# Performance work log

Hardware: AMD Instinct MI355X
Metric: run time of the kernel (lower is better)

The kernel has to match this reference:

```python
import jax, jax.numpy as jnp
import numpy as np

B, K, P, T = 4096, 128, 64, 4

def setup_inputs() -> dict:
    key = jax.random.key(0)
    ks = jax.random.split(key, 9)
    s = lambda k, shp: jax.random.normal(k, shp, dtype=jnp.float32) * 0.1
    return {
        "x": jax.random.normal(ks[0], (B, K, 1), dtype=jnp.float32),
        "w": jax.random.normal(ks[1], (B, K, 1), dtype=jnp.float32),
        "W1": s(ks[2], (P, 1)),   # theta_1: 1 -> p
        "W2": s(ks[3], (P, P)),   # theta_2: p -> p
        "W3": s(ks[4], (P, P)),   # theta_3: p -> p
        "W4": s(ks[5], (P, 1)),   # theta_4: 1 -> p
        "W5": s(ks[6], (1, 2 * P)),  # theta_5: 2p -> 1
        "W6": s(ks[7], (P, P)),   # theta_6: p -> p
        "W7": s(ks[8], (P, P)),   # theta_7: p -> p
    }


def reference(x, w, W1, W2, W3, W4, W5, W6, W7):
    # x, w: (B, K, 1). torch Linear(in,out,bias=False): y = v @ W.T, W: (out,in)
    b, k, _ = x.shape
    p = W1.shape[0]
    # per-node feature messages (invariant across T iterations in original code)
    tmsg = jax.nn.relu(jnp.einsum('bki,pi->bkp', w, W4))   # relu(theta_4(w_k)), (B,K,p)
    sum_t = tmsg.sum(axis=1, keepdims=True)                # (B,1,p)
    xmsg = jnp.einsum('bki,pi->bkp', x, W1)                # theta_1(x_k), (B,K,p)
    mu = jnp.zeros((b, k, p), dtype=x.dtype)
    for _ in range(T):
        sum_mu = mu.sum(axis=1, keepdims=True)             # (B,1,p)
        mu = jax.nn.relu(
            xmsg
            + jnp.einsum('bkp,qp->bkq', sum_mu - mu, W2)   # theta_2(sum_mu - mu_k)
            + jnp.einsum('bkp,qp->bkq', sum_t - tmsg, W3)  # theta_3(sum_t - t_k)
        )
    pooled = jax.nn.relu(jnp.einsum('bp,qp->bq', mu.sum(axis=1), W6))  # (B,p)
    local = jnp.einsum('bkp,qp->bkq', mu, W7)                           # (B,K,p)
    # theta_5(concat(relu(theta_6(pool)), theta_7(mu_k))); split W5 = [W5a | W5b]
    W5a, W5b = W5[:, :p], W5[:, p:]
    q = jnp.einsum('bp,op->bo', pooled, W5a)[:, None, :] + jnp.einsum('bkp,op->bko', local, W5b)
    return q  # (B, K, 1)
```

## Files before the change

### kernel.cpp

```cpp
#include <hip/hip_runtime.h>

typedef __bf16 bf16;
typedef __bf16 bf16x4 __attribute__((ext_vector_type(4)));
typedef __bf16 bf16x8 __attribute__((ext_vector_type(8)));
typedef float  f32x4  __attribute__((ext_vector_type(4)));

#define MFMA16(a, b, c) __builtin_amdgcn_mfma_f32_16x16x32_bf16((a), (b), (c), 0, 0, 0)

__global__ __launch_bounds__(64, 2)
void qnet_kernel(const float* __restrict__ Xg, const float* __restrict__ Wg,
                 const float* __restrict__ W1g, const float* __restrict__ W2g,
                 const float* __restrict__ W3g, const float* __restrict__ W4g,
                 const float* __restrict__ W5g, const float* __restrict__ W6g,
                 const float* __restrict__ W7g, float* __restrict__ Outg)
{
    __shared__ __align__(16) bf16 muS[128 * 64];
    __shared__ __align__(16) float uS[64];
    __shared__ __align__(16) float smS[64];

    const int lane = threadIdx.x;
    const int b    = blockIdx.x;
    const int l15  = lane & 15;
    const int quad = lane >> 4;
    const int sw   = l15 & 7;

    float xv0 = Xg[b * 128 + lane], xv1 = Xg[b * 128 + 64 + lane];
    float wv0 = Wg[b * 128 + lane], wv1 = Wg[b * 128 + 64 + lane];

    float Ap = fmaxf(wv0, 0.f) + fmaxf(wv1, 0.f);
    float Bn = fmaxf(-wv0, 0.f) + fmaxf(-wv1, 0.f);
#pragma unroll
    for (int m = 1; m < 64; m <<= 1) { Ap += __shfl_xor(Ap, m); Bn += __shfl_xor(Bn, m); }

    float xk[8], apk[8], bnk[8];
#pragma unroll
    for (int kt = 0; kt < 8; ++kt) {
        const int src = (kt & 3) * 16 + l15;
        float xs_ = (kt < 4) ? __shfl(xv0, src) : __shfl(xv1, src);
        float ws_ = (kt < 4) ? __shfl(wv0, src) : __shfl(wv1, src);
        xk[kt]  = xs_;
        apk[kt] = Ap - fmaxf(ws_, 0.f);
        bnk[kt] = Bn - fmaxf(-ws_, 0.f);
    }

    float sp = 0.f, sm = 0.f;
#pragma unroll
    for (int c = 0; c < 16; ++c) {
        f32x4 w4 = *(const f32x4*)&W4g[c * 4];
        f32x4 w3 = *(const f32x4*)&W3g[lane * 64 + c * 4];
#pragma unroll
        for (int e = 0; e < 4; ++e) {
            sp += fmaxf(w4[e], 0.f) * w3[e];
            sm += fmaxf(-w4[e], 0.f) * w3[e];
        }
    }
    float w1C[16], v3pC[16], v3mC[16];
#pragma unroll
    for (int qt = 0; qt < 4; ++qt) {
        f32x4 w1v = *(const f32x4*)&W1g[qt * 16 + quad * 4];
#pragma unroll
        for (int e = 0; e < 4; ++e) {
            const int q = qt * 16 + quad * 4 + e;
            v3pC[qt * 4 + e] = __shfl(sp, q);
            v3mC[qt * 4 + e] = __shfl(sm, q);
            w1C[qt * 4 + e]  = w1v[e];
        }
    }

    {
        float u = 0.f;
#pragma unroll
        for (int c = 0; c < 16; ++c) {
            f32x4 w5v = *(const f32x4*)&W5g[64 + c * 4];
#pragma unroll
            for (int e = 0; e < 4; ++e) u += w5v[e] * W7g[(c * 4 + e) * 64 + lane];
        }
        uS[lane] = u;
    }

    bf16x8 w2h[4][2], w2l[4][2];
#pragma unroll
    for (int qt = 0; qt < 4; ++qt)
#pragma unroll
        for (int s = 0; s < 2; ++s) {
            const float* src = &W2g[(qt * 16 + l15) * 64 + s * 32 + quad * 8];
            f32x4 f0 = *(const f32x4*)src;
            f32x4 f1 = *(const f32x4*)(src + 4);
            bf16x8 h, l;
#pragma unroll
            for (int e = 0; e < 4; ++e) {
                bf16 h0 = (bf16)f0[e], h1 = (bf16)f1[e];
                h[e] = h0; h[4 + e] = h1;
                l[e]     = (bf16)(f0[e] - (float)h0);
                l[4 + e] = (bf16)(f1[e] - (float)h1);
            }
            w2h[qt][s] = h; w2l[qt][s] = l;
        }

#pragma unroll
    for (int kt = 0; kt < 8; ++kt) {
        const int row = (kt * 16 + l15) * 64;
#pragma unroll
        for (int qt = 0; qt < 4; ++qt) {
            bf16x4 h;
#pragma unroll
            for (int e = 0; e < 4; ++e) {
                float t = fmaf(xk[kt], w1C[qt * 4 + e],
                          fmaf(apk[kt], v3pC[qt * 4 + e], bnk[kt] * v3mC[qt * 4 + e]));
                h[e] = (bf16)fmaxf(t, 0.f);
            }
            *(bf16x4*)&muS[row + ((2 * qt + (quad >> 1)) ^ sw) * 8 + 4 * (quad & 1)] = h;
        }
    }

    const f32x4 zero4 = {0.f, 0.f, 0.f, 0.f};
    float smv[16];
#pragma unroll
    for (int i = 0; i < 16; ++i) smv[i] = 0.f;

    for (int it = 0; it < 3; ++it) {
        f32x4 rs[4] = {zero4, zero4, zero4, zero4};
#pragma unroll
        for (int kt = 0; kt < 8; ++kt) {
            const int row = (kt * 16 + l15) * 64;
            bf16x8 m0 = *(const bf16x8*)&muS[row + ((quad) ^ sw) * 8];
            bf16x8 m1 = *(const bf16x8*)&muS[row + ((4 + quad) ^ sw) * 8];
#pragma unroll
            for (int qt = 0; qt < 4; ++qt) {
                f32x4 a = MFMA16(w2h[qt][0], m0, zero4);
                a = MFMA16(w2h[qt][1], m1, a);
                f32x4 c = MFMA16(w2l[qt][0], m0, zero4);
                c = MFMA16(w2l[qt][1], m1, c);
                rs[qt] += a + c;
            }
        }
#pragma unroll
        for (int m = 1; m <= 8; m <<= 1)
#pragma unroll
            for (int qt = 0; qt < 4; ++qt)
#pragma unroll
                for (int e = 0; e < 4; ++e)
                    rs[qt][e] += __shfl_xor(rs[qt][e], m);

#pragma unroll
        for (int kt = 0; kt < 8; ++kt) {
            const int row = (kt * 16 + l15) * 64;
            bf16x8 m0 = *(const bf16x8*)&muS[row + ((quad) ^ sw) * 8];
            bf16x8 m1 = *(const bf16x8*)&muS[row + ((4 + quad) ^ sw) * 8];
#pragma unroll
            for (int qt = 0; qt < 4; ++qt) {
                f32x4 a = MFMA16(w2h[qt][0], m0, zero4);
                a = MFMA16(w2h[qt][1], m1, a);
                bf16x4 h;
#pragma unroll
                for (int e = 0; e < 4; ++e) {
                    float t = fmaf(xk[kt], w1C[qt * 4 + e], rs[qt][e]);
                    t = fmaf(apk[kt], v3pC[qt * 4 + e], t);
                    t = fmaf(bnk[kt], v3mC[qt * 4 + e], t);
                    float v = fmaxf(t - a[e], 0.f);
                    h[e] = (bf16)v;
                    if (it == 2) smv[qt * 4 + e] += v;
                }
                *(bf16x4*)&muS[row + ((2 * qt + (quad >> 1)) ^ sw) * 8 + 4 * (quad & 1)] = h;
            }
        }
    }

#pragma unroll
    for (int m = 1; m <= 8; m <<= 1)
#pragma unroll
        for (int i = 0; i < 16; ++i) smv[i] += __shfl_xor(smv[i], m);
    if (l15 == 0) {
#pragma unroll
        for (int qt = 0; qt < 4; ++qt) {
            f32x4 v = {smv[qt * 4], smv[qt * 4 + 1], smv[qt * 4 + 2], smv[qt * 4 + 3]};
            *(f32x4*)&smS[qt * 16 + quad * 4] = v;
        }
    }

    float pl = 0.f;
#pragma unroll
    for (int c = 0; c < 16; ++c) {
        f32x4 sv = *(const f32x4*)&smS[c * 4];
        f32x4 w6 = *(const f32x4*)&W6g[lane * 64 + c * 4];
#pragma unroll
        for (int e = 0; e < 4; ++e) pl = fmaf(sv[e], w6[e], pl);
    }
    float qa = fmaxf(pl, 0.f) * W5g[lane];
#pragma unroll
    for (int m = 1; m < 64; m <<= 1) qa += __shfl_xor(qa, m);

    f32x4 uf[2][2];
#pragma unroll
    for (int s = 0; s < 2; ++s) {
        uf[s][0] = *(const f32x4*)&uS[s * 32 + quad * 8];
        uf[s][1] = *(const f32x4*)&uS[s * 32 + quad * 8 + 4];
    }

    float res[8];
#pragma unroll
    for (int kt = 0; kt < 8; ++kt) {
        const int row = (kt * 16 + l15) * 64;
        bf16x8 m0 = *(const bf16x8*)&muS[row + ((quad) ^ sw) * 8];
        bf16x8 m1 = *(const bf16x8*)&muS[row + ((4 + quad) ^ sw) * 8];
        float r = 0.f;
#pragma unroll
        for (int j = 0; j < 4; ++j) {
            r = fmaf((float)m0[j],     uf[0][0][j], r);
            r = fmaf((float)m0[4 + j], uf[0][1][j], r);
            r = fmaf((float)m1[j],     uf[1][0][j], r);
            r = fmaf((float)m1[4 + j], uf[1][1][j], r);
        }
        r += __shfl_xor(r, 16); r += __shfl_xor(r, 32);
        res[kt] = r;
    }
    float rA0 = (quad & 1) ? res[1] : res[0];
    float rA1 = (quad & 1) ? res[3] : res[2];
    float rA  = (quad & 2) ? rA1 : rA0;
    float rB0 = (quad & 1) ? res[5] : res[4];
    float rB1 = (quad & 1) ? res[7] : res[6];
    float rB  = (quad & 2) ? rB1 : rB0;
    Outg[b * 128 + lane]      = qa + rA;
    Outg[b * 128 + 64 + lane] = qa + rB;
}

extern "C" void kernel_launch(void* const* d_in, const int* in_sizes, int n_in,
                              void* d_out, int out_size, void* d_ws, size_t ws_size,
                              hipStream_t stream) {
    (void)n_in; (void)d_ws; (void)ws_size; (void)out_size;
    const int B = in_sizes[0] >> 7;
    qnet_kernel<<<B, 64, 0, stream>>>(
        (const float*)d_in[0], (const float*)d_in[1], (const float*)d_in[2],
        (const float*)d_in[3], (const float*)d_in[4], (const float*)d_in[5],
        (const float*)d_in[6], (const float*)d_in[7], (const float*)d_in[8],
        (float*)d_out);
}
```

Before: 136.3 us.

## Process two batch elements per wavefront to amortize weight setup and interleave MFMAs

Each single-wavefront block now handles two batch items. The per-block weight preprocessing (W2 hi/lo split into registers, W3/W4 folds, W7·W5b vector) is paid once per pair, and the MFMA chains for the two items are interleaved to expose more independent work. The cost is double the LDS use per block, more live registers, and half as many blocks, which reduces the wavefronts available to hide latency. Launch bounds are relaxed to allow the larger register footprint, and the launch assumes B is even.

```diff
diff --git a/kernel.cpp b/kernel.cpp
--- a/kernel.cpp
+++ b/kernel.cpp
@@ -7,40 +7,42 @@
 
 #define MFMA16(a, b, c) __builtin_amdgcn_mfma_f32_16x16x32_bf16((a), (b), (c), 0, 0, 0)
 
-__global__ __launch_bounds__(64, 2)
+__global__ __launch_bounds__(64, 1)
 void qnet_kernel(const float* __restrict__ Xg, const float* __restrict__ Wg,
                  const float* __restrict__ W1g, const float* __restrict__ W2g,
                  const float* __restrict__ W3g, const float* __restrict__ W4g,
                  const float* __restrict__ W5g, const float* __restrict__ W6g,
                  const float* __restrict__ W7g, float* __restrict__ Outg)
 {
-    __shared__ __align__(16) bf16 muS[128 * 64];
+    __shared__ __align__(16) bf16 muS[2][128 * 64];
     __shared__ __align__(16) float uS[64];
-    __shared__ __align__(16) float smS[64];
+    __shared__ __align__(16) float smS[2][64];
 
     const int lane = threadIdx.x;
-    const int b    = blockIdx.x;
+    const int b0   = blockIdx.x * 2;
     const int l15  = lane & 15;
     const int quad = lane >> 4;
     const int sw   = l15 & 7;
 
-    float xv0 = Xg[b * 128 + lane], xv1 = Xg[b * 128 + 64 + lane];
-    float wv0 = Wg[b * 128 + lane], wv1 = Wg[b * 128 + 64 + lane];
-
-    float Ap = fmaxf(wv0, 0.f) + fmaxf(wv1, 0.f);
-    float Bn = fmaxf(-wv0, 0.f) + fmaxf(-wv1, 0.f);
-#pragma unroll
-    for (int m = 1; m < 64; m <<= 1) { Ap += __shfl_xor(Ap, m); Bn += __shfl_xor(Bn, m); }
-
-    float xk[8], apk[8], bnk[8];
-#pragma unroll
-    for (int kt = 0; kt < 8; ++kt) {
-        const int src = (kt & 3) * 16 + l15;
-        float xs_ = (kt < 4) ? __shfl(xv0, src) : __shfl(xv1, src);
-        float ws_ = (kt < 4) ? __shfl(wv0, src) : __shfl(wv1, src);
-        xk[kt]  = xs_;
-        apk[kt] = Ap - fmaxf(ws_, 0.f);
-        bnk[kt] = Bn - fmaxf(-ws_, 0.f);
+    float xk[2][8], apk[2][8], bnk[2][8];
+#pragma unroll
+    for (int u = 0; u < 2; ++u) {
+        const int b = b0 + u;
+        float xv0 = Xg[b * 128 + lane], xv1 = Xg[b * 128 + 64 + lane];
+        float wv0 = Wg[b * 128 + lane], wv1 = Wg[b * 128 + 64 + lane];
+        float Ap = fmaxf(wv0, 0.f) + fmaxf(wv1, 0.f);
+        float Bn = fmaxf(-wv0, 0.f) + fmaxf(-wv1, 0.f);
+#pragma unroll
+        for (int m = 1; m < 64; m <<= 1) { Ap += __shfl_xor(Ap, m); Bn += __shfl_xor(Bn, m); }
+#pragma unroll
+        for (int kt = 0; kt < 8; ++kt) {
+            const int src = (kt & 3) * 16 + l15;
+            float xs_ = (kt < 4) ? __shfl(xv0, src) : __shfl(xv1, src);
+            float ws_ = (kt < 4) ? __shfl(wv0, src) : __shfl(wv1, src);
+            xk[u][kt]  = xs_;
+            apk[u][kt] = Ap - fmaxf(ws_, 0.f);
+            bnk[u][kt] = Bn - fmaxf(-ws_, 0.f);
+        }
     }
 
     float sp = 0.f, sm = 0.f;
@@ -101,37 +103,44 @@
     for (int kt = 0; kt < 8; ++kt) {
         const int row = (kt * 16 + l15) * 64;
 #pragma unroll
-        for (int qt = 0; qt < 4; ++qt) {
-            bf16x4 h;
-#pragma unroll
-            for (int e = 0; e < 4; ++e) {
-                float t = fmaf(xk[kt], w1C[qt * 4 + e],
-                          fmaf(apk[kt], v3pC[qt * 4 + e], bnk[kt] * v3mC[qt * 4 + e]));
-                h[e] = (bf16)fmaxf(t, 0.f);
-            }
-            *(bf16x4*)&muS[row + ((2 * qt + (quad >> 1)) ^ sw) * 8 + 4 * (quad & 1)] = h;
-        }
+        for (int u = 0; u < 2; ++u)
+#pragma unroll
+            for (int qt = 0; qt < 4; ++qt) {
+                bf16x4 h;
+#pragma unroll
+                for (int e = 0; e < 4; ++e) {
+                    float t = fmaf(xk[u][kt], w1C[qt * 4 + e],
+                              fmaf(apk[u][kt], v3pC[qt * 4 + e], bnk[u][kt] * v3mC[qt * 4 + e]));
+                    h[e] = (bf16)fmaxf(t, 0.f);
+                }
+                *(bf16x4*)&muS[u][row + ((2 * qt + (quad >> 1)) ^ sw) * 8 + 4 * (quad & 1)] = h;
+            }
     }
 
     const f32x4 zero4 = {0.f, 0.f, 0.f, 0.f};
-    float smv[16];
-#pragma unroll
-    for (int i = 0; i < 16; ++i) smv[i] = 0.f;
-
+    float smv[2][16];
     for (int it = 0; it < 3; ++it) {
-        f32x4 rs[4] = {zero4, zero4, zero4, zero4};
+        f32x4 rs0[4] = {zero4, zero4, zero4, zero4};
+        f32x4 rs1[4] = {zero4, zero4, zero4, zero4};
 #pragma unroll
         for (int kt = 0; kt < 8; ++kt) {
             const int row = (kt * 16 + l15) * 64;
-            bf16x8 m0 = *(const bf16x8*)&muS[row + ((quad) ^ sw) * 8];
-            bf16x8 m1 = *(const bf16x8*)&muS[row + ((4 + quad) ^ sw) * 8];
-#pragma unroll
-            for (int qt = 0; qt < 4; ++qt) {
-                f32x4 a = MFMA16(w2h[qt][0], m0, zero4);
-                a = MFMA16(w2h[qt][1], m1, a);
-                f32x4 c = MFMA16(w2l[qt][0], m0, zero4);
-                c = MFMA16(w2l[qt][1], m1, c);
-                rs[qt] += a + c;
+            bf16x8 a0 = *(const bf16x8*)&muS[0][row + ((quad) ^ sw) * 8];
+            bf16x8 a1 = *(const bf16x8*)&muS[0][row + ((4 + quad) ^ sw) * 8];
+            bf16x8 b0v = *(const bf16x8*)&muS[1][row + ((quad) ^ sw) * 8];
+            bf16x8 b1v = *(const bf16x8*)&muS[1][row + ((4 + quad) ^ sw) * 8];
+#pragma unroll
+            for (int qt = 0; qt < 4; ++qt) {
+                f32x4 pa = MFMA16(w2h[qt][0], a0, zero4);
+                pa = MFMA16(w2h[qt][1], a1, pa);
+                f32x4 qa_ = MFMA16(w2l[qt][0], a0, zero4);
+                qa_ = MFMA16(w2l[qt][1], a1, qa_);
+                rs0[qt] += pa + qa_;
+                f32x4 pb = MFMA16(w2h[qt][0], b0v, zero4);
+                pb = MFMA16(w2h[qt][1], b1v, pb);
+                f32x4 qb = MFMA16(w2l[qt][0], b0v, zero4);
+                qb = MFMA16(w2l[qt][1], b1v, qb);
+                rs1[qt] += pb + qb;
             }
         }
 #pragma unroll
@@ -139,29 +148,42 @@
 #pragma unroll
             for (int qt = 0; qt < 4; ++qt)
 #pragma unroll
-                for (int e = 0; e < 4; ++e)
-                    rs[qt][e] += __shfl_xor(rs[qt][e], m);
+                for (int e = 0; e < 4; ++e) {
+                    rs0[qt][e] += __shfl_xor(rs0[qt][e], m);
+                    rs1[qt][e] += __shfl_xor(rs1[qt][e], m);
+                }
 
 #pragma unroll
         for (int kt = 0; kt < 8; ++kt) {
             const int row = (kt * 16 + l15) * 64;
-            bf16x8 m0 = *(const bf16x8*)&muS[row + ((quad) ^ sw) * 8];
-            bf16x8 m1 = *(const bf16x8*)&muS[row + ((4 + quad) ^ sw) * 8];
-#pragma unroll
-            for (int qt = 0; qt < 4; ++qt) {
-                f32x4 a = MFMA16(w2h[qt][0], m0, zero4);
-                a = MFMA16(w2h[qt][1], m1, a);
-                bf16x4 h;
+            bf16x8 a0 = *(const bf16x8*)&muS[0][row + ((quad) ^ sw) * 8];
+            bf16x8 a1 = *(const bf16x8*)&muS[0][row + ((4 + quad) ^ sw) * 8];
+            bf16x8 b0v = *(const bf16x8*)&muS[1][row + ((quad) ^ sw) * 8];
+            bf16x8 b1v = *(const bf16x8*)&muS[1][row + ((4 + quad) ^ sw) * 8];
+#pragma unroll
+            for (int qt = 0; qt < 4; ++qt) {
+                f32x4 aa = MFMA16(w2h[qt][0], a0, zero4);
+                aa = MFMA16(w2h[qt][1], a1, aa);
+                f32x4 ab = MFMA16(w2h[qt][0], b0v, zero4);
+                ab = MFMA16(w2h[qt][1], b1v, ab);
+                bf16x4 ha, hb;
 #pragma unroll
                 for (int e = 0; e < 4; ++e) {
-                    float t = fmaf(xk[kt], w1C[qt * 4 + e], rs[qt][e]);
-                    t = fmaf(apk[kt], v3pC[qt * 4 + e], t);
-                    t = fmaf(bnk[kt], v3mC[qt * 4 + e], t);
-                    float v = fmaxf(t - a[e], 0.f);
-                    h[e] = (bf16)v;
-                    if (it == 2) smv[qt * 4 + e] += v;
+                    float t = fmaf(xk[0][kt], w1C[qt * 4 + e], rs0[qt][e]);
+                    t = fmaf(apk[0][kt], v3pC[qt * 4 + e], t);
+                    t = fmaf(bnk[0][kt], v3mC[qt * 4 + e], t);
+                    float v = fmaxf(t - aa[e], 0.f);
+                    ha[e] = (bf16)v;
+                    float t2 = fmaf(xk[1][kt], w1C[qt * 4 + e], rs1[qt][e]);
+                    t2 = fmaf(apk[1][kt], v3pC[qt * 4 + e], t2);
+                    t2 = fmaf(bnk[1][kt], v3mC[qt * 4 + e], t2);
+                    float v2 = fmaxf(t2 - ab[e], 0.f);
+                    hb[e] = (bf16)v2;
+                    if (it == 2) { smv[0][qt * 4 + e] = (kt == 0 ? v : smv[0][qt * 4 + e] + v);
+                                   smv[1][qt * 4 + e] = (kt == 0 ? v2 : smv[1][qt * 4 + e] + v2); }
                 }
-                *(bf16x4*)&muS[row + ((2 * qt + (quad >> 1)) ^ sw) * 8 + 4 * (quad & 1)] = h;
+                *(bf16x4*)&muS[0][row + ((2 * qt + (quad >> 1)) ^ sw) * 8 + 4 * (quad & 1)] = ha;
+                *(bf16x4*)&muS[1][row + ((2 * qt + (quad >> 1)) ^ sw) * 8 + 4 * (quad & 1)] = hb;
             }
         }
     }
@@ -169,26 +191,34 @@
 #pragma unroll
     for (int m = 1; m <= 8; m <<= 1)
 #pragma unroll
-        for (int i = 0; i < 16; ++i) smv[i] += __shfl_xor(smv[i], m);
+        for (int i = 0; i < 16; ++i) {
+            smv[0][i] += __shfl_xor(smv[0][i], m);
+            smv[1][i] += __shfl_xor(smv[1][i], m);
+        }
     if (l15 == 0) {
 #pragma unroll
-        for (int qt = 0; qt < 4; ++qt) {
-            f32x4 v = {smv[qt * 4], smv[qt * 4 + 1], smv[qt * 4 + 2], smv[qt * 4 + 3]};
-            *(f32x4*)&smS[qt * 16 + quad * 4] = v;
-        }
-    }
-
-    float pl = 0.f;
+        for (int u = 0; u < 2; ++u)
+#pragma unroll
+            for (int qt = 0; qt < 4; ++qt) {
+                f32x4 v = {smv[u][qt * 4], smv[u][qt * 4 + 1], smv[u][qt * 4 + 2], smv[u][qt * 4 + 3]};
+                *(f32x4*)&smS[u][qt * 16 + quad * 4] = v;
+            }
+    }
+
+    float pl0 = 0.f, pl1 = 0.f;
 #pragma unroll
     for (int c = 0; c < 16; ++c) {
-        f32x4 sv = *(const f32x4*)&smS[c * 4];
+        f32x4 sv0 = *(const f32x4*)&smS[0][c * 4];
+        f32x4 sv1 = *(const f32x4*)&smS[1][c * 4];
         f32x4 w6 = *(const f32x4*)&W6g[lane * 64 + c * 4];
 #pragma unroll
-        for (int e = 0; e < 4; ++e) pl = fmaf(sv[e], w6[e], pl);
-    }
-    float qa = fmaxf(pl, 0.f) * W5g[lane];
-#pragma unroll
-    for (int m = 1; m < 64; m <<= 1) qa += __shfl_xor(qa, m);
+        for (int e = 0; e < 4; ++e) { pl0 = fmaf(sv0[e], w6[e], pl0); pl1 = fmaf(sv1[e], w6[e], pl1); }
+    }
+    float w5a = W5g[lane];
+    float qa0 = fmaxf(pl0, 0.f) * w5a;
+    float qa1 = fmaxf(pl1, 0.f) * w5a;
+#pragma unroll
+    for (int m = 1; m < 64; m <<= 1) { qa0 += __shfl_xor(qa0, m); qa1 += __shfl_xor(qa1, m); }
 
     f32x4 uf[2][2];
 #pragma unroll
@@ -197,31 +227,35 @@
         uf[s][1] = *(const f32x4*)&uS[s * 32 + quad * 8 + 4];
     }
 
-    float res[8];
-#pragma unroll
-    for (int kt = 0; kt < 8; ++kt) {
-        const int row = (kt * 16 + l15) * 64;
-        bf16x8 m0 = *(const bf16x8*)&muS[row + ((quad) ^ sw) * 8];
-        bf16x8 m1 = *(const bf16x8*)&muS[row + ((4 + quad) ^ sw) * 8];
-        float r = 0.f;
-#pragma unroll
-        for (int j = 0; j < 4; ++j) {
-            r = fmaf((float)m0[j],     uf[0][0][j], r);
-            r = fmaf((float)m0[4 + j], uf[0][1][j], r);
-            r = fmaf((float)m1[j],     uf[1][0][j], r);
-            r = fmaf((float)m1[4 + j], uf[1][1][j], r);
-        }
-        r += __shfl_xor(r, 16); r += __shfl_xor(r, 32);
-        res[kt] = r;
-    }
-    float rA0 = (quad & 1) ? res[1] : res[0];
-    float rA1 = (quad & 1) ? res[3] : res[2];
-    float rA  = (quad & 2) ? rA1 : rA0;
-    float rB0 = (quad & 1) ? res[5] : res[4];
-    float rB1 = (quad & 1) ? res[7] : res[6];
-    float rB  = (quad & 2) ? rB1 : rB0;
-    Outg[b * 128 + lane]      = qa + rA;
-    Outg[b * 128 + 64 + lane] = qa + rB;
+#pragma unroll
+    for (int u = 0; u < 2; ++u) {
+        float res[8];
+#pragma unroll
+        for (int kt = 0; kt < 8; ++kt) {
+            const int row = (kt * 16 + l15) * 64;
+            bf16x8 m0 = *(const bf16x8*)&muS[u][row + ((quad) ^ sw) * 8];
+            bf16x8 m1 = *(const bf16x8*)&muS[u][row + ((4 + quad) ^ sw) * 8];
+            float r = 0.f;
+#pragma unroll
+            for (int j = 0; j < 4; ++j) {
+                r = fmaf((float)m0[j],     uf[0][0][j], r);
+                r = fmaf((float)m0[4 + j], uf[0][1][j], r);
+                r = fmaf((float)m1[j],     uf[1][0][j], r);
+                r = fmaf((float)m1[4 + j], uf[1][1][j], r);
+            }
+            r += __shfl_xor(r, 16); r += __shfl_xor(r, 32);
+            res[kt] = r;
+        }
+        float rA0 = (quad & 1) ? res[1] : res[0];
+        float rA1 = (quad & 1) ? res[3] : res[2];
+        float rA  = (quad & 2) ? rA1 : rA0;
+        float rB0 = (quad & 1) ? res[5] : res[4];
+        float rB1 = (quad & 1) ? res[7] : res[6];
+        float rB  = (quad & 2) ? rB1 : rB0;
+        float qa = u ? qa1 : qa0;
+        Outg[(b0 + u) * 128 + lane]      = qa + rA;
+        Outg[(b0 + u) * 128 + 64 + lane] = qa + rB;
+    }
 }
 
 extern "C" void kernel_launch(void* const* d_in, const int* in_sizes, int n_in,
@@ -229,7 +263,7 @@
                               hipStream_t stream) {
     (void)n_in; (void)d_ws; (void)ws_size; (void)out_size;
     const int B = in_sizes[0] >> 7;
-    qnet_kernel<<<B, 64, 0, stream>>>(
+    qnet_kernel<<<B / 2, 64, 0, stream>>>(
         (const float*)d_in[0], (const float*)d_in[1], (const float*)d_in[2],
         (const float*)d_in[3], (const float*)d_in[4], (const float*)d_in[5],
         (const float*)d_in[6], (const float*)d_in[7], (const float*)d_in[8],
```

Measured after the change: 164.9 us. 1.21x slower.
